# Optimization experiments

Measured on AMD Instinct MI355X. Metric: run time of the kernel, lower is better.

The kernel has to match this reference:

```python
import jax, jax.numpy as jnp
import numpy as np

B, SQ, SKV, D, H = 2, 2048, 2048, 1024, 16
HD = D // H  # 64
SIGMOID_BIAS = -8.0
LN_EPS = 1e-5


def setup_inputs() -> dict:
    key = jax.random.key(0)
    ks = jax.random.split(key, 6)
    s = D ** -0.5
    return {
        "q": jax.random.normal(ks[0], (B, SQ, D), dtype=jnp.float32),
        "kv": jax.random.normal(ks[1], (B, SKV, D), dtype=jnp.float32),
        "Wq": jax.random.normal(ks[2], (D, D), dtype=jnp.float32) * s,
        "Wkv": jax.random.normal(ks[3], (D, 2 * D), dtype=jnp.float32) * s,
        "v_gamma": jnp.ones((HD,), dtype=jnp.float32),
        "v_beta": jnp.zeros((HD,), dtype=jnp.float32),
        "Wproj": jax.random.normal(ks[4], (D, D), dtype=jnp.float32) * s,
    }


def _layernorm(x, gamma, beta):
    # LayerNorm over the last dim (head_dim)
    mu = jnp.mean(x, axis=-1, keepdims=True)
    var = jnp.mean(jnp.square(x - mu), axis=-1, keepdims=True)
    return (x - mu) * jax.lax.rsqrt(var + LN_EPS) * gamma + beta


def reference(q, kv, Wq, Wkv, v_gamma, v_beta, Wproj):
    # Projections (no bias)
    qh = (q @ Wq).reshape(B, SQ, H, HD)                    # [B,Sq,H,hd]
    kvh = (kv @ Wkv).reshape(B, SKV, 2, H, HD)
    k = kvh[:, :, 0]                                       # [B,Skv,H,hd]
    v = kvh[:, :, 1]
    # v_norm is always applied (qk_norm=False -> q/k norms are identity)
    v = _layernorm(v, v_gamma, v_beta)
    # prescale: scale both q and k by head_dim ** -0.25
    scale = HD ** -0.25
    logits = jnp.einsum("bqhd,bkhd->bhqk", qh * scale, k * scale)
    # sigmoid attention (no softmax normalization), causal mask:
    # score masked where i + Skv - Sq - j < 0  <=>  j > i (equal lengths)
    iq = jnp.arange(SQ)[:, None]
    jk = jnp.arange(SKV)[None, :]
    causal_mask = (jk <= iq + (SKV - SQ)).astype(logits.dtype)  # [Sq,Skv]
    attn = jax.nn.sigmoid(logits + SIGMOID_BIAS) * causal_mask
    attn_times_v = jnp.einsum("bhqk,bkhd->bqhd", attn, v).reshape(B, SQ, D)
    attn_proj = attn_times_v @ Wproj
    return attn_times_v, attn_proj
```

## Files before the change

### kernel.cpp

```cpp
#include <hip/hip_runtime.h>
#include <hip/hip_bf16.h>

#define B_ 2
#define SQ_ 2048
#define SKV_ 2048
#define D_ 1024
#define H_ 16
#define HD_ 64

typedef unsigned short u16;
typedef float f32x4 __attribute__((ext_vector_type(4)));
typedef float f32x16 __attribute__((ext_vector_type(16)));
typedef short s16x8 __attribute__((ext_vector_type(8)));

__device__ __forceinline__ u16 f2bf(float f) {
  union { float f; unsigned u; } v; v.f = f;
  return (u16)((v.u + 0x7FFFu + ((v.u >> 16) & 1u)) >> 16);
}
__device__ __forceinline__ u16 f2bf_fast(float f) {
  union { float f; unsigned u; } v; v.f = f;
  return (u16)((v.u + 0x8000u) >> 16);
}
__device__ __forceinline__ float bf2f(u16 h) {
  union { unsigned u; float f; } v; v.u = ((unsigned)h) << 16;
  return v.f;
}
__device__ __forceinline__ f32x4 mfma16(s16x8 a, s16x8 b, f32x4 c) {
  return __builtin_amdgcn_mfma_f32_16x16x32_bf16(a, b, c, 0, 0, 0);
}
__device__ __forceinline__ f32x16 mfma32(s16x8 a, s16x8 b, f32x16 c) {
  return __builtin_amdgcn_mfma_f32_32x32x16_bf16(a, b, c, 0, 0, 0);
}
__device__ __forceinline__ void async16(const u16* g, u16* l) {
  __builtin_amdgcn_global_load_lds(
      (const __attribute__((address_space(1))) unsigned int*)g,
      (__attribute__((address_space(3))) unsigned int*)l, 16, 0, 0);
}

__device__ __forceinline__ void tr_tile(const float* __restrict__ in, u16* __restrict__ out,
                                        int R, int C, int cx, int ry, int t) {
  __shared__ u16 tile[32][33];
  int tx = t & 31, ty = t >> 5;
  int c0 = cx * 32, r0 = ry * 32;
#pragma unroll
  for (int i = 0; i < 4; i++)
    tile[ty + i * 8][tx] = f2bf(in[(size_t)(r0 + ty + i * 8) * C + c0 + tx]);
  __syncthreads();
#pragma unroll
  for (int i = 0; i < 4; i++)
    out[(size_t)(c0 + ty + i * 8) * R + r0 + tx] = tile[tx][ty + i * 8];
}

__device__ __forceinline__ void cast4(const float* __restrict__ in, u16* __restrict__ out,
                                      int i) {
  float4 f = *(const float4*)(in + i);
  ushort4 o;
  o.x = f2bf(f.x); o.y = f2bf(f.y); o.z = f2bf(f.z); o.w = f2bf(f.w);
  *(ushort4*)(out + i) = o;
}

__global__ __launch_bounds__(256) void prep_kernel(
    const float* __restrict__ q, u16* __restrict__ q_bf,
    const float* __restrict__ kv, u16* __restrict__ kv_bf,
    const float* __restrict__ Wq, u16* __restrict__ WqT,
    const float* __restrict__ Wkv, u16* __restrict__ WkvT,
    const float* __restrict__ Wproj, u16* __restrict__ WprT) {
  int bid = blockIdx.x, t = threadIdx.x;
  if (bid < 4096) {
    cast4(q, q_bf, bid * 1024 + t * 4);
  } else if (bid < 8192) {
    cast4(kv, kv_bf, (bid - 4096) * 1024 + t * 4);
  } else if (bid < 9216) {
    int b2 = bid - 8192;
    tr_tile(Wq, WqT, 1024, 1024, b2 & 31, b2 >> 5, t);
  } else if (bid < 11264) {
    int b2 = bid - 9216;
    tr_tile(Wkv, WkvT, 1024, 2048, b2 & 63, b2 >> 6, t);
  } else {
    int b2 = bid - 11264;
    tr_tile(Wproj, WprT, 1024, 1024, b2 & 31, b2 >> 5, t);
  }
}

template <int BM, int BN, bool OUT_BF16>
__device__ __forceinline__ void gemm_body(const u16* __restrict__ A,
                                          const u16* __restrict__ BT,
                                          void* __restrict__ Cout,
                                          int m0, int n0, int N, int K) {
  __shared__ __attribute__((aligned(16))) u16 As[BM][32];
  __shared__ __attribute__((aligned(16))) u16 Bs[BN][32];
  constexpr int AM = BM / 32, AN = BN / 32;
  int t = threadIdx.x, w = t >> 6, lane = t & 63;
  int l16 = lane & 15, quad = lane >> 4;
  int mw = (w >> 1) * (BM / 2), nw = (w & 1) * (BN / 2);
  int grow = w * 16 + (lane >> 2);
  int gcol = (lane & 3) * 8;

  f32x4 acc[AM][AN] = {};

  for (int kt = 0; kt < K; kt += 32) {
    __syncthreads();
#pragma unroll
    for (int j = 0; j < BM / 64; j++)
      async16(A + (size_t)(m0 + j * 64 + grow) * K + kt + gcol, &As[j * 64 + w * 16][0]);
#pragma unroll
    for (int j = 0; j < BN / 64; j++)
      async16(BT + (size_t)(n0 + j * 64 + grow) * K + kt + gcol, &Bs[j * 64 + w * 16][0]);
    __syncthreads();
    s16x8 af[AM], bf[AN];
#pragma unroll
    for (int i = 0; i < AM; i++) af[i] = *(const s16x8*)&As[mw + i * 16 + l16][quad * 8];
#pragma unroll
    for (int j = 0; j < AN; j++) bf[j] = *(const s16x8*)&Bs[nw + j * 16 + l16][quad * 8];
#pragma unroll
    for (int i = 0; i < AM; i++)
#pragma unroll
      for (int j = 0; j < AN; j++)
        acc[i][j] = mfma16(af[i], bf[j], acc[i][j]);
  }

#pragma unroll
  for (int i = 0; i < AM; i++)
#pragma unroll
    for (int j = 0; j < AN; j++) {
      int col = n0 + nw + j * 16 + l16;
#pragma unroll
      for (int r = 0; r < 4; r++) {
        int row = m0 + mw + i * 16 + quad * 4 + r;
        float v = acc[i][j][r];
        if (OUT_BF16)
          ((u16*)Cout)[(size_t)row * N + col] = f2bf(v);
        else
          ((float*)Cout)[(size_t)row * N + col] = v;
      }
    }
}

__global__ __launch_bounds__(256, 3) void gemm_qkv(const u16* __restrict__ q_bf,
                                                   const u16* __restrict__ WqT,
                                                   u16* __restrict__ qh,
                                                   const u16* __restrict__ kv_bf,
                                                   const u16* __restrict__ WkvT,
                                                   u16* __restrict__ kvh) {
  int bx = blockIdx.x;
  if (bx < 8)
    gemm_body<128, 128, true>(q_bf, WqT, qh, blockIdx.y * 128, bx * 128, D_, D_);
  else
    gemm_body<128, 128, true>(kv_bf, WkvT, kvh, blockIdx.y * 128, (bx - 8) * 128, 2 * D_, D_);
}

__global__ __launch_bounds__(256, 3) void gemm_proj(const u16* __restrict__ A,
                                                    const u16* __restrict__ BT,
                                                    float* __restrict__ C) {
  gemm_body<64, 128, false>(A, BT, C, blockIdx.y * 64, blockIdx.x * 128, D_, D_);
}

__global__ __launch_bounds__(256) void ln_vt_kernel(const u16* __restrict__ kvh,
                                                    const float* __restrict__ gamma,
                                                    const float* __restrict__ beta,
                                                    u16* __restrict__ vt) {
  __shared__ __attribute__((aligned(16))) u16 tile[64][72];
  int bid = blockIdx.x;
  int stile = bid & 31;
  int h = (bid >> 5) & 15;
  int b = bid >> 9;
  int wave = threadIdx.x >> 6, lane = threadIdx.x & 63;
  float g = gamma[lane], be = beta[lane];
#pragma unroll 4
  for (int i = 0; i < 16; i++) {
    int s = stile * 64 + wave * 16 + i;
    float x = bf2f(kvh[(size_t)(b * SKV_ + s) * 2048 + 1024 + h * 64 + lane]);
    float sum = x;
#pragma unroll
    for (int off = 32; off; off >>= 1) sum += __shfl_xor(sum, off, 64);
    float mu = sum * (1.0f / 64.0f);
    float dx = x - mu;
    float s2 = dx * dx;
#pragma unroll
    for (int off = 32; off; off >>= 1) s2 += __shfl_xor(s2, off, 64);
    float inv = rsqrtf(s2 * (1.0f / 64.0f) + 1e-5f);
    tile[lane][wave * 16 + i] = f2bf(dx * inv * g + be);
  }
  __syncthreads();
  int d = threadIdx.x >> 2, sc = (threadIdx.x & 3) * 16;
  size_t orow = ((size_t)(b * H_ + h) * 64 + d) * SKV_ + stile * 64 + sc;
  uint4 v0 = *(const uint4*)&tile[d][sc];
  uint4 v1 = *(const uint4*)&tile[d][sc + 8];
  *(uint4*)(vt + orow) = v0;
  *(uint4*)(vt + orow + 8) = v1;
}

__global__ __launch_bounds__(256, 1) void attn_kernel(const u16* __restrict__ qh,
                                                      const u16* __restrict__ kvh,
                                                      const u16* __restrict__ vt,
                                                      float* __restrict__ out0,
                                                      u16* __restrict__ atv_bf) {
  __shared__ __attribute__((aligned(16))) u16 Ks[2][64][72];
  __shared__ __attribute__((aligned(16))) u16 Vs[2][64][72];
  __shared__ __attribute__((aligned(16))) u16 Ps[4][32][72];

  int bh = blockIdx.x;
  int pair = blockIdx.y;
  int h = bh & 15, b = bh >> 4;
  int t = threadIdx.x;
  int w = t >> 6, lane = t & 63;
  int l31 = lane & 31, hi = lane >> 5;
  int srow = t >> 2;
  int scol = (t & 3) * 16;

  const float C1 = -0.18033688011f;
  const float C2 = 11.5415603272f;

  const u16* gkb = kvh + ((size_t)(b * SKV_) + srow) * 2048 + h * 64 + scol;
  const u16* gvb = vt + ((size_t)((b * H_ + h) * 64 + srow)) * 2048 + scol;

  for (int half = 0; half < 2; half++) {
    int qt = half ? (15 - pair) : pair;
    int q0 = qt * 128;
    int nkv = 2 * qt + 2;

    s16x8 qf[4];
    {
      const u16* qp = qh + (size_t)(b * SQ_ + q0 + w * 32 + l31) * D_ + h * 64 + hi * 8;
#pragma unroll
      for (int c = 0; c < 4; c++) qf[c] = *(const s16x8*)(qp + c * 16);
    }

    f32x16 oacc[2] = {};

    uint4 kr0 = *(const uint4*)gkb, kr1 = *(const uint4*)(gkb + 8);
    uint4 vr0 = *(const uint4*)gvb, vr1 = *(const uint4*)(gvb + 8);

    for (int kt = 0; kt < nkv; kt++) {
      int buf = kt & 1;
      *(uint4*)&Ks[buf][srow][scol] = kr0; *(uint4*)&Ks[buf][srow][scol + 8] = kr1;
      *(uint4*)&Vs[buf][srow][scol] = vr0; *(uint4*)&Vs[buf][srow][scol + 8] = vr1;
      __syncthreads();
      if (kt + 1 < nkv) {
        const u16* gk2 = gkb + (size_t)(kt + 1) * 64 * 2048;
        const u16* gv2 = gvb + (size_t)(kt + 1) * 64;
        kr0 = *(const uint4*)gk2; kr1 = *(const uint4*)(gk2 + 8);
        vr0 = *(const uint4*)gv2; vr1 = *(const uint4*)(gv2 + 8);
      }

      int kk0 = kt * 64;
      bool need_mask = (kt >= 2 * qt);
      int qi = q0 + w * 32 + l31;

#pragma unroll
      for (int ktile = 0; ktile < 2; ktile++) {
        f32x16 st = {};
#pragma unroll
        for (int c = 0; c < 4; c++) {
          s16x8 kf = *(const s16x8*)&Ks[buf][ktile * 32 + l31][c * 16 + hi * 8];
          st = mfma32(kf, qf[c], st);
        }
#pragma unroll
        for (int g = 0; g < 4; g++) {
          unsigned lo, hi2;
          u16 pk[4];
#pragma unroll
          for (int i = 0; i < 4; i++) {
            float s = st[4 * g + i];
            float e = __builtin_amdgcn_exp2f(s * C1 + C2);
            float p = __builtin_amdgcn_rcpf(1.0f + e);
            if (need_mask) {
              int kj = kk0 + ktile * 32 + 8 * g + 4 * hi + i;
              if (kj > qi) p = 0.0f;
            }
            pk[i] = f2bf_fast(p);
          }
          lo = (unsigned)pk[0] | ((unsigned)pk[1] << 16);
          hi2 = (unsigned)pk[2] | ((unsigned)pk[3] << 16);
          uint2 pv; pv.x = lo; pv.y = hi2;
          *(uint2*)&Ps[w][l31][ktile * 32 + 8 * g + 4 * hi] = pv;
        }
      }

      s16x8 pa[4];
#pragma unroll
      for (int kc = 0; kc < 4; kc++)
        pa[kc] = *(const s16x8*)&Ps[w][l31][kc * 16 + hi * 8];
#pragma unroll
      for (int dt = 0; dt < 2; dt++)
#pragma unroll
        for (int kc = 0; kc < 4; kc++) {
          s16x8 vf = *(const s16x8*)&Vs[buf][dt * 32 + l31][kc * 16 + hi * 8];
          oacc[dt] = mfma32(pa[kc], vf, oacc[dt]);
        }
    }

#pragma unroll
    for (int dt = 0; dt < 2; dt++)
#pragma unroll
      for (int reg = 0; reg < 16; reg++) {
        int ql = (reg & 3) + 8 * (reg >> 2) + 4 * hi;
        int row = q0 + w * 32 + ql;
        int col = h * 64 + dt * 32 + l31;
        size_t idx = (size_t)(b * SQ_ + row) * D_ + col;
        float v = oacc[dt][reg];
        out0[idx] = v;
        atv_bf[idx] = f2bf(v);
      }
    __syncthreads();
  }
}

extern "C" void kernel_launch(void* const* d_in, const int* in_sizes, int n_in,
                              void* d_out, int out_size, void* d_ws, size_t ws_size,
                              hipStream_t stream) {
  const float* q      = (const float*)d_in[0];
  const float* kv     = (const float*)d_in[1];
  const float* Wq     = (const float*)d_in[2];
  const float* Wkv    = (const float*)d_in[3];
  const float* vgamma = (const float*)d_in[4];
  const float* vbeta  = (const float*)d_in[5];
  const float* Wproj  = (const float*)d_in[6];
  float* out0 = (float*)d_out;
  float* out1 = out0 + (size_t)B_ * SQ_ * D_;

  char* p = (char*)d_ws;
  u16* q_bf  = (u16*)p; p += (size_t)B_ * SQ_ * D_ * 2;
  u16* kv_bf = (u16*)p; p += (size_t)B_ * SKV_ * D_ * 2;
  u16* WqT   = (u16*)p; p += (size_t)D_ * D_ * 2;
  u16* WkvT  = (u16*)p; p += (size_t)2 * D_ * D_ * 2;
  u16* WprT  = (u16*)p; p += (size_t)D_ * D_ * 2;
  u16* qh    = (u16*)p; p += (size_t)B_ * SQ_ * D_ * 2;
  u16* kvh   = (u16*)p; p += (size_t)B_ * SKV_ * 2 * D_ * 2;
  u16* vt    = (u16*)p; p += (size_t)B_ * H_ * HD_ * SKV_ * 2;
  u16* atv   = (u16*)p; p += (size_t)B_ * SQ_ * D_ * 2;

  prep_kernel<<<dim3(12288), 256, 0, stream>>>(q, q_bf, kv, kv_bf, Wq, WqT, Wkv, WkvT, Wproj, WprT);

  gemm_qkv<<<dim3(24, 32), 256, 0, stream>>>(q_bf, WqT, qh, kv_bf, WkvT, kvh);

  ln_vt_kernel<<<dim3((B_ * H_ * SKV_) / 64), 256, 0, stream>>>(kvh, vgamma, vbeta, vt);

  attn_kernel<<<dim3(32, 8), 256, 0, stream>>>(qh, kvh, vt, out0, atv);

  gemm_proj<<<dim3(8, 64), 256, 0, stream>>>(atv, WprT, out1);
}
```

Before: 216.5 us.

## Split attention into 64-row query tiles with a KV split across waves

The query tile shrinks from 128 to 64 rows, which doubles the grid to 512 blocks while keeping the causal pairing of tiles. The four waves are now arranged as 2 query slices times 2 KV halves, and the two partial outputs are combined through LDS scratch that reuses the K buffer. Causal masking is applied only on the diagonal KV tile, launch bounds allow 2 blocks per CU, and LDS row padding is shrunk. The aim is better CU occupancy and load balance, paid for by an extra cross-wave reduction and synchronisations. The new padding also leaves some 16-byte LDS accesses unaligned.

New measurement: 204.5 us. 1.06x faster.

```diff
diff --git a/kernel.cpp b/kernel.cpp
--- a/kernel.cpp
+++ b/kernel.cpp
@@ -190,14 +190,14 @@
   *(uint4*)(vt + orow + 8) = v1;
 }
 
-__global__ __launch_bounds__(256, 1) void attn_kernel(const u16* __restrict__ qh,
+__global__ __launch_bounds__(256, 2) void attn_kernel(const u16* __restrict__ qh,
                                                       const u16* __restrict__ kvh,
                                                       const u16* __restrict__ vt,
                                                       float* __restrict__ out0,
                                                       u16* __restrict__ atv_bf) {
-  __shared__ __attribute__((aligned(16))) u16 Ks[2][64][72];
-  __shared__ __attribute__((aligned(16))) u16 Vs[2][64][72];
-  __shared__ __attribute__((aligned(16))) u16 Ps[4][32][72];
+  __shared__ __attribute__((aligned(16))) u16 Ks[2][64][68];
+  __shared__ __attribute__((aligned(16))) u16 Vs[2][64][68];
+  __shared__ __attribute__((aligned(16))) u16 Ps[4][32][36];
 
   int bh = blockIdx.x;
   int pair = blockIdx.y;
@@ -205,6 +205,7 @@
   int t = threadIdx.x;
   int w = t >> 6, lane = t & 63;
   int l31 = lane & 31, hi = lane >> 5;
+  int qs = w & 1, kh = w >> 1;
   int srow = t >> 2;
   int scol = (t & 3) * 16;
 
@@ -213,15 +214,16 @@
 
   const u16* gkb = kvh + ((size_t)(b * SKV_) + srow) * 2048 + h * 64 + scol;
   const u16* gvb = vt + ((size_t)((b * H_ + h) * 64 + srow)) * 2048 + scol;
+  float* Osc = (float*)&Ks[0][0][0];
 
   for (int half = 0; half < 2; half++) {
-    int qt = half ? (15 - pair) : pair;
-    int q0 = qt * 128;
-    int nkv = 2 * qt + 2;
+    int qt = half ? (31 - pair) : pair;
+    int q0 = qt * 64;
+    int nkv = qt + 1;
 
     s16x8 qf[4];
     {
-      const u16* qp = qh + (size_t)(b * SQ_ + q0 + w * 32 + l31) * D_ + h * 64 + hi * 8;
+      const u16* qp = qh + (size_t)(b * SQ_ + q0 + qs * 32 + l31) * D_ + h * 64 + hi * 8;
 #pragma unroll
       for (int c = 0; c < 4; c++) qf[c] = *(const s16x8*)(qp + c * 16);
     }
@@ -243,65 +245,87 @@
         vr0 = *(const uint4*)gv2; vr1 = *(const uint4*)(gv2 + 8);
       }
 
-      int kk0 = kt * 64;
-      bool need_mask = (kt >= 2 * qt);
-      int qi = q0 + w * 32 + l31;
-
-#pragma unroll
-      for (int ktile = 0; ktile < 2; ktile++) {
-        f32x16 st = {};
-#pragma unroll
-        for (int c = 0; c < 4; c++) {
-          s16x8 kf = *(const s16x8*)&Ks[buf][ktile * 32 + l31][c * 16 + hi * 8];
-          st = mfma32(kf, qf[c], st);
-        }
+      f32x16 st = {};
+#pragma unroll
+      for (int c = 0; c < 4; c++) {
+        s16x8 kf = *(const s16x8*)&Ks[buf][kh * 32 + l31][c * 16 + hi * 8];
+        st = mfma32(kf, qf[c], st);
+      }
+
+      if (kt == nkv - 1) {
+        int qi = q0 + qs * 32 + l31;
+        int kbase = kt * 64 + kh * 32 + 4 * hi;
 #pragma unroll
         for (int g = 0; g < 4; g++) {
-          unsigned lo, hi2;
           u16 pk[4];
 #pragma unroll
           for (int i = 0; i < 4; i++) {
             float s = st[4 * g + i];
             float e = __builtin_amdgcn_exp2f(s * C1 + C2);
             float p = __builtin_amdgcn_rcpf(1.0f + e);
-            if (need_mask) {
-              int kj = kk0 + ktile * 32 + 8 * g + 4 * hi + i;
-              if (kj > qi) p = 0.0f;
-            }
+            if (kbase + 8 * g + i > qi) p = 0.0f;
             pk[i] = f2bf_fast(p);
           }
-          lo = (unsigned)pk[0] | ((unsigned)pk[1] << 16);
-          hi2 = (unsigned)pk[2] | ((unsigned)pk[3] << 16);
-          uint2 pv; pv.x = lo; pv.y = hi2;
-          *(uint2*)&Ps[w][l31][ktile * 32 + 8 * g + 4 * hi] = pv;
+          uint2 pv;
+          pv.x = (unsigned)pk[0] | ((unsigned)pk[1] << 16);
+          pv.y = (unsigned)pk[2] | ((unsigned)pk[3] << 16);
+          *(uint2*)&Ps[w][l31][8 * g + 4 * hi] = pv;
+        }
+      } else {
+#pragma unroll
+        for (int g = 0; g < 4; g++) {
+          u16 pk[4];
+#pragma unroll
+          for (int i = 0; i < 4; i++) {
+            float s = st[4 * g + i];
+            float e = __builtin_amdgcn_exp2f(s * C1 + C2);
+            pk[i] = f2bf_fast(__builtin_amdgcn_rcpf(1.0f + e));
+          }
+          uint2 pv;
+          pv.x = (unsigned)pk[0] | ((unsigned)pk[1] << 16);
+          pv.y = (unsigned)pk[2] | ((unsigned)pk[3] << 16);
+          *(uint2*)&Ps[w][l31][8 * g + 4 * hi] = pv;
         }
       }
 
-      s16x8 pa[4];
-#pragma unroll
-      for (int kc = 0; kc < 4; kc++)
+      s16x8 pa[2];
+#pragma unroll
+      for (int kc = 0; kc < 2; kc++)
         pa[kc] = *(const s16x8*)&Ps[w][l31][kc * 16 + hi * 8];
 #pragma unroll
       for (int dt = 0; dt < 2; dt++)
 #pragma unroll
-        for (int kc = 0; kc < 4; kc++) {
-          s16x8 vf = *(const s16x8*)&Vs[buf][dt * 32 + l31][kc * 16 + hi * 8];
+        for (int kc = 0; kc < 2; kc++) {
+          s16x8 vf = *(const s16x8*)&Vs[buf][dt * 32 + l31][kh * 32 + kc * 16 + hi * 8];
           oacc[dt] = mfma32(pa[kc], vf, oacc[dt]);
         }
     }
 
-#pragma unroll
-    for (int dt = 0; dt < 2; dt++)
-#pragma unroll
-      for (int reg = 0; reg < 16; reg++) {
-        int ql = (reg & 3) + 8 * (reg >> 2) + 4 * hi;
-        int row = q0 + w * 32 + ql;
-        int col = h * 64 + dt * 32 + l31;
-        size_t idx = (size_t)(b * SQ_ + row) * D_ + col;
-        float v = oacc[dt][reg];
-        out0[idx] = v;
-        atv_bf[idx] = f2bf(v);
-      }
+    __syncthreads();
+    if (kh == 1) {
+#pragma unroll
+      for (int dt = 0; dt < 2; dt++)
+#pragma unroll
+        for (int reg = 0; reg < 16; reg++) {
+          int ql = (reg & 3) + 8 * (reg >> 2) + 4 * hi;
+          Osc[(qs * 32 + ql) * 66 + dt * 32 + l31] = oacc[dt][reg];
+        }
+    }
+    __syncthreads();
+    if (kh == 0) {
+#pragma unroll
+      for (int dt = 0; dt < 2; dt++)
+#pragma unroll
+        for (int reg = 0; reg < 16; reg++) {
+          int ql = (reg & 3) + 8 * (reg >> 2) + 4 * hi;
+          float v = oacc[dt][reg] + Osc[(qs * 32 + ql) * 66 + dt * 32 + l31];
+          int row = q0 + qs * 32 + ql;
+          int col = h * 64 + dt * 32 + l31;
+          size_t idx = (size_t)(b * SQ_ + row) * D_ + col;
+          out0[idx] = v;
+          atv_bf[idx] = f2bf(v);
+        }
+    }
     __syncthreads();
   }
 }
@@ -336,7 +360,7 @@
 
   ln_vt_kernel<<<dim3((B_ * H_ * SKV_) / 64), 256, 0, stream>>>(kvh, vgamma, vbeta, vt);
 
-  attn_kernel<<<dim3(32, 8), 256, 0, stream>>>(qh, kvh, vt, out0, atv);
+  attn_kernel<<<dim3(32, 16), 256, 0, stream>>>(qh, kvh, vt, out0, atv);
 
   gemm_proj<<<dim3(8, 64), 256, 0, stream>>>(atv, WprT, out1);
 }
```
